# Kernel optimization log

Measured on AMD Instinct MI355X. Metric: run time of the kernel, lower is better.

The kernel has to match this reference:

```python
import jax, jax.numpy as jnp
import numpy as np

K = 4
TEMPERATURE = 30.0


def setup_inputs() -> dict:
    key = jax.random.key(0)
    ks = jax.random.split(key, 6)
    B, C, H, W_sp = 32, 128, 56, 56
    Cout, kh, kw = 128, 3, 3
    Cred = max(C // 4, 1)
    x = jax.random.normal(ks[0], (B, C, H, W_sp), dtype=jnp.float32)
    # K parallel conv kernels + biases (fan-in scaled init)
    fan = C * kh * kw
    W = jax.random.normal(ks[1], (K, Cout, C, kh, kw), dtype=jnp.float32) / np.sqrt(fan)
    b = jax.random.normal(ks[2], (K, Cout), dtype=jnp.float32) * 0.01
    # attention branch: 1x1 convs == dense on pooled features
    aw1 = jax.random.normal(ks[3], (Cred, C), dtype=jnp.float32) / np.sqrt(C)
    aw2 = jax.random.normal(ks[4], (K, Cred), dtype=jnp.float32) / np.sqrt(Cred)
    return {"x": x, "W": W, "b": b, "aw1": aw1, "aw2": aw2}


def reference(x, W, b, aw1, aw2):
    # attention: global avg pool -> 1x1 conv (dense) -> relu -> 1x1 conv -> softmax(logits/T)
    pooled = jnp.mean(x, axis=(2, 3))                       # [B, C]
    h1 = jax.nn.relu(jnp.einsum('bc,rc->br', pooled, aw1))  # [B, Cred]
    logits = jnp.einsum('br,kr->bk', h1, aw2)               # [B, K]
    attn = jax.nn.softmax(logits / TEMPERATURE, axis=1)     # [B, K]

    pad = 1
    out = None
    for i in range(K):  # fixed small K, structurally distinct kernels
        yi = jax.lax.conv_general_dilated(
            x, W[i], window_strides=(1, 1), padding=[(pad, pad), (pad, pad)],
            dimension_numbers=('NCHW', 'OIHW', 'NCHW'))
        yi = yi + b[i][None, :, None, None]
        yi = yi * attn[:, i][:, None, None, None]
        out = yi if out is None else out + yi
    return out
```

## Files before the change

kernel.cpp:

```cpp
#include <hip/hip_runtime.h>
#include <hip/hip_bf16.h>
#include <stdint.h>

typedef __bf16 bf16x8 __attribute__((ext_vector_type(8)));
typedef float  f32x4  __attribute__((ext_vector_type(4)));
typedef unsigned short u16x8 __attribute__((ext_vector_type(8)));
typedef unsigned int   u32x4 __attribute__((ext_vector_type(4)));

#define NB 32
#define NC 128
#define NH 56
#define NW 56
#define NK 4
#define NCO 128
#define NCR 32
#define NHW 3136
#define TEMPER 30.0f

#define WS_ATTN   0u
#define WS_BC     4096u
#define WS_ROWSUM 65536u
#define WS_WC     1048576u
#define WS_XT     10485760u

__global__ void xt_kernel(const float* __restrict__ x, __hip_bfloat16* __restrict__ xt,
                          float* __restrict__ rowsum) {
  __shared__ float lds[58 * 133];
  int xcd = blockIdx.x & 7;
  int j   = blockIdx.x >> 3;
  int b   = xcd * 4 + j / 58;
  int hp  = j % 58;
  int blk = b * 58 + hp;
  int h = hp - 1;
  bool hin = (h >= 0) && (h < NH);
  int tid = threadIdx.x;
  if (hin) {
    const float* xrow = x + ((size_t)b * NC) * NHW + (size_t)h * NW;
    for (int i = tid; i < 128 * 14; i += 256) {
      int c = i / 14;
      int w4 = (i - c * 14) * 4;
      float4 v = *(const float4*)(xrow + (size_t)c * NHW + w4);
      int base = (w4 + 1) * 133 + c;
      lds[base]         = v.x;
      lds[base + 133]   = v.y;
      lds[base + 2*133] = v.z;
      lds[base + 3*133] = v.w;
    }
  }
  __syncthreads();
  __hip_bfloat16* orow = xt + (size_t)blk * (58 * 128);
  for (int i = tid; i < 58 * 16; i += 256) {
    int wp = i >> 4;
    int cg = (i & 15) << 3;
    u16x8 o;
    if (!hin || wp == 0 || wp == 57) {
      o = (u16x8)0;
    } else {
      const float* src = lds + wp * 133 + cg;
      #pragma unroll
      for (int jx = 0; jx < 8; ++jx) {
        union { __hip_bfloat16 b; unsigned short u; } cv;
        cv.b = __float2bfloat16(src[jx]);
        o[jx] = cv.u;
      }
    }
    *(u16x8*)(orow + wp * 128 + cg) = o;
  }
  if (hin && tid < 128) {
    float s = 0.f;
    #pragma unroll 8
    for (int wp = 1; wp <= 56; ++wp) s += lds[wp * 133 + tid];
    rowsum[(size_t)blk * 128 + tid] = s;
  }
}

__global__ void attn_kernel(const float* __restrict__ rowsum, const float* __restrict__ aw1,
                            const float* __restrict__ aw2, const float* __restrict__ bias,
                            float* __restrict__ attn, float* __restrict__ bc_out) {
  int b = blockIdx.x;
  __shared__ float sp[NC], h1[NCR], at[NK];
  int t = threadIdx.x;
  if (t < NC) {
    float s = 0.f;
    for (int hp = 1; hp <= 56; ++hp) s += rowsum[((size_t)b * 58 + hp) * 128 + t];
    sp[t] = s * (1.0f / (float)NHW);
  }
  __syncthreads();
  if (t < NCR) {
    float s = 0.f;
    for (int c = 0; c < NC; ++c) s += aw1[t*NC + c] * sp[c];
    h1[t] = s > 0.f ? s : 0.f;
  }
  __syncthreads();
  if (t == 0) {
    float lg[NK], mx = -1e30f;
    for (int k = 0; k < NK; ++k) {
      float s = 0.f;
      for (int r = 0; r < NCR; ++r) s += aw2[k*NCR + r] * h1[r];
      lg[k] = s * (1.0f/TEMPER);
      mx = fmaxf(mx, lg[k]);
    }
    float den = 0.f, e[NK];
    for (int k = 0; k < NK; ++k) { e[k] = expf(lg[k]-mx); den += e[k]; }
    float inv = 1.0f/den;
    for (int k = 0; k < NK; ++k) { at[k] = e[k]*inv; attn[b*NK+k] = at[k]; }
  }
  __syncthreads();
  if (t < NCO) {
    float s = 0.f;
    for (int k = 0; k < NK; ++k) s += at[k] * bias[k*NCO + t];
    bc_out[b*NCO + t] = s;
  }
}

__global__ void combine_kernel(const float* __restrict__ W, const float* __restrict__ attn,
                               __hip_bfloat16* __restrict__ wc) {
  int gid = blockIdx.x;
  int bg  = gid >> 6;
  int tcell = (gid & 63) * 256 + threadIdx.x;
  int co = tcell >> 7, ci = tcell & 127;
  float w[4][9];
  const float* wp = W + ((size_t)co * 128 + ci) * 9;
  #pragma unroll
  for (int k = 0; k < 4; ++k)
    #pragma unroll
    for (int j = 0; j < 9; ++j)
      w[k][j] = wp[(size_t)k * 147456 + j];
  for (int b = bg * 8; b < bg * 8 + 8; ++b) {
    float a0 = attn[b*4+0], a1 = attn[b*4+1], a2 = attn[b*4+2], a3 = attn[b*4+3];
    #pragma unroll
    for (int j = 0; j < 9; ++j) {
      float v = a0*w[0][j] + a1*w[1][j] + a2*w[2][j] + a3*w[3][j];
      wc[(((size_t)b*9 + j) * 128 + co) * 128 + ci] = __float2bfloat16(v);
    }
  }
}

#define RS 2368
#define CS 40
#define BBUF (3072*8)
#define ABUF (1536*8)

__global__ __launch_bounds__(512, 2) void conv_kernel(
    const unsigned short* __restrict__ xt,
    const unsigned short* __restrict__ wc,
    const float* __restrict__ bc,
    float* __restrict__ out) {
  __shared__ __align__(16) unsigned short lds_a[2*ABUF];
  __shared__ __align__(16) unsigned short lds_b[2*BBUF];
  const int tid  = threadIdx.x;
  const int lane = tid & 63;
  const int wv   = tid >> 6;
  const int wm   = wv >> 2;
  const int wn   = wv & 3;
  const int bid  = blockIdx.x;
  const int xcd  = bid & 7;
  const int jj   = bid >> 3;
  const int b    = xcd*4 + jj/7;
  const int r0   = (jj % 7) * 8;
  const int li   = lane & 15;
  const int kg   = lane >> 4;

  int srcB[6];
  #pragma unroll
  for (int i = 0; i < 6; ++i) {
    int q = i*512 + tid;
    int r = q / 296;
    int sl = q - r*296;
    int col = sl / 5;
    int part = sl - col*5;
    int rc = r  > 9  ? 9  : r;
    int cl = col > 57 ? 57 : col;
    int pc = part > 3 ? 3 : part;
    srcB[i] = ((r0 + rc)*58 + cl)*128 + pc*8;
  }
  int srcA[3];
  #pragma unroll
  for (int i = 0; i < 3; ++i) {
    int c = i*512 + tid;
    int kwl  = c >> 9;
    int co   = (c & 511) >> 2;
    int part = c & 3;
    srcA[i] = (kwl*128 + co)*128 + part*8;
  }

  int xoff[7];
  #pragma unroll
  for (int f = 0; f < 7; ++f) {
    int pos = wn*112 + f*16 + li;
    int rB = pos / 56;
    int cB = pos - rB*56;
    xoff[f] = rB*RS + cB*CS + kg*8;
  }
  const int aRead = (wm*64 + li)*32 + kg*8;

  const f32x4 vzero = {0.f, 0.f, 0.f, 0.f};
  f32x4 acc[4][7];
  #pragma unroll
  for (int mo = 0; mo < 4; ++mo)
    #pragma unroll
    for (int f = 0; f < 7; ++f) acc[mo][f] = vzero;

  const unsigned short* xtg = xt + (size_t)b*(58*58*128);
  const unsigned short* wcg = wc + (size_t)b*(9*128*128);

  u32x4 aST[3], bST[6];

  #define LOAD_A(ccn, khn) do { \
    _Pragma("unroll") \
    for (int i = 0; i < 3; ++i) \
      aST[i] = *(const u32x4*)(wcg + (khn)*49152 + srcA[i] + (ccn)*32); \
  } while (0)

  #define LOAD_B(ccn) do { \
    _Pragma("unroll") \
    for (int i = 0; i < 6; ++i) \
      bST[i] = *(const u32x4*)(xtg + srcB[i] + (ccn)*32); \
  } while (0)

  #define WRITE_A(bufidx) do { \
    _Pragma("unroll") \
    for (int i = 0; i < 3; ++i) \
      *(u32x4*)(lds_a + (bufidx)*ABUF + (i*512 + tid)*8) = aST[i]; \
  } while (0)

  #define WRITE_B(bufidx) do { \
    _Pragma("unroll") \
    for (int i = 0; i < 6; ++i) \
      *(u32x4*)(lds_b + (bufidx)*BBUF + (i*512 + tid)*8) = bST[i]; \
  } while (0)

  #define COMPUTE(s, cc, kh) do { \
    const unsigned short* pa = lds_a + ((s)&1)*ABUF; \
    const unsigned short* pb = lds_b + ((cc)&1)*BBUF; \
    _Pragma("unroll") \
    for (int kwl = 0; kwl < 3; ++kwl) { \
      bf16x8 af[4], bf[7]; \
      _Pragma("unroll") \
      for (int mo = 0; mo < 4; ++mo) \
        af[mo] = *(const bf16x8*)(pa + kwl*4096 + aRead + mo*512); \
      _Pragma("unroll") \
      for (int f = 0; f < 7; ++f) \
        bf[f] = *(const bf16x8*)(pb + xoff[f] + (kh)*RS + kwl*CS); \
      __builtin_amdgcn_s_setprio(1); \
      _Pragma("unroll") \
      for (int mo = 0; mo < 4; ++mo) \
        _Pragma("unroll") \
        for (int f = 0; f < 7; ++f) \
          acc[mo][f] = __builtin_amdgcn_mfma_f32_16x16x32_bf16(af[mo], bf[f], acc[mo][f], 0, 0, 0); \
      __builtin_amdgcn_s_setprio(0); \
    } \
  } while (0)

  #define STEP(s, cc, kh) do { \
    if ((s) < 11) LOAD_A(((s)+1)/3, ((s)+1)%3); \
    if ((kh) == 0 && (cc) < 3) LOAD_B((cc)+1); \
    COMPUTE(s, cc, kh); \
    __syncthreads(); \
    if ((s) < 11) WRITE_A(((s)+1)&1); \
    if ((kh) == 0 && (cc) < 3) WRITE_B(((cc)+1)&1); \
    __syncthreads(); \
  } while (0)

  LOAD_A(0, 0);
  LOAD_B(0);
  WRITE_A(0);
  WRITE_B(0);
  __syncthreads();

  STEP(0,  0, 0);
  STEP(1,  0, 1);
  STEP(2,  0, 2);
  STEP(3,  1, 0);
  STEP(4,  1, 1);
  STEP(5,  1, 2);
  STEP(6,  2, 0);
  STEP(7,  2, 1);
  STEP(8,  2, 2);
  STEP(9,  3, 0);
  STEP(10, 3, 1);
  STEP(11, 3, 2);

  float* ob = out + (size_t)b*NCO*NHW;
  #pragma unroll
  for (int mo = 0; mo < 4; ++mo) {
    #pragma unroll
    for (int rg = 0; rg < 4; ++rg) {
      const int co = wm*64 + mo*16 + kg*4 + rg;
      const float bv = bc[b*NCO + co];
      float* orow = ob + (size_t)co*NHW;
      #pragma unroll
      for (int f = 0; f < 7; ++f) {
        int pos = wn*112 + f*16 + li;
        int rB = pos / 56;
        int cB = pos - rB*56;
        orow[(r0 + rB)*56 + cB] = acc[mo][f][rg] + bv;
      }
    }
  }
}

extern "C" void kernel_launch(void* const* d_in, const int* in_sizes, int n_in,
                              void* d_out, int out_size, void* d_ws, size_t ws_size,
                              hipStream_t stream) {
  const float* x   = (const float*)d_in[0];
  const float* W   = (const float*)d_in[1];
  const float* bia = (const float*)d_in[2];
  const float* aw1 = (const float*)d_in[3];
  const float* aw2 = (const float*)d_in[4];
  float* out = (float*)d_out;
  char* ws = (char*)d_ws;
  float* attn   = (float*)(ws + WS_ATTN);
  float* bcm    = (float*)(ws + WS_BC);
  float* rowsum = (float*)(ws + WS_ROWSUM);
  __hip_bfloat16* wc = (__hip_bfloat16*)(ws + WS_WC);
  __hip_bfloat16* xt = (__hip_bfloat16*)(ws + WS_XT);

  xt_kernel<<<NB*58, 256, 0, stream>>>(x, xt, rowsum);
  attn_kernel<<<NB, 128, 0, stream>>>(rowsum, aw1, aw2, bia, attn, bcm);
  combine_kernel<<<256, 256, 0, stream>>>(W, attn, wc);
  conv_kernel<<<224, 512, 0, stream>>>((const unsigned short*)xt,
                                       (const unsigned short*)wc, bcm, out);
}
```

Before: 67.41 us.

## Add producer warps staging tiles via global_load_lds for warp-specialized conv

Adds two dedicated producer wavefronts to the conv block. They copy weight and input tiles straight from global memory into LDS using global_load_lds, while the 8 compute wavefronts only run MFMA. This removes the register round-trip and the extra barrier that the old design spent staging loads through VGPRs. The cost is that only 2 waves handle all loads, there is one sync per step, and launch bounds change to 640 threads with one block per CU, which may lower occupancy.

New measurement: 110.8 us. +64.4%, slower.

```diff
diff --git a/kernel.cpp b/kernel.cpp
--- a/kernel.cpp
+++ b/kernel.cpp
@@ -5,7 +5,6 @@
 typedef __bf16 bf16x8 __attribute__((ext_vector_type(8)));
 typedef float  f32x4  __attribute__((ext_vector_type(4)));
 typedef unsigned short u16x8 __attribute__((ext_vector_type(8)));
-typedef unsigned int   u32x4 __attribute__((ext_vector_type(4)));
 
 #define NB 32
 #define NC 128
@@ -138,10 +137,15 @@
 
 #define RS 2368
 #define CS 40
-#define BBUF (3072*8)
-#define ABUF (1536*8)
-
-__global__ __launch_bounds__(512, 2) void conv_kernel(
+#define ABUF 12288
+#define BBUF 24576
+
+#define GLOAD16(src, dst) \
+  __builtin_amdgcn_global_load_lds( \
+    (const __attribute__((address_space(1))) unsigned int*)(src), \
+    (__attribute__((address_space(3))) unsigned int*)(dst), 16, 0, 0)
+
+__global__ __launch_bounds__(640, 1) void conv_kernel(
     const unsigned short* __restrict__ xt,
     const unsigned short* __restrict__ wc,
     const float* __restrict__ bc,
@@ -151,8 +155,6 @@
   const int tid  = threadIdx.x;
   const int lane = tid & 63;
   const int wv   = tid >> 6;
-  const int wm   = wv >> 2;
-  const int wn   = wv & 3;
   const int bid  = blockIdx.x;
   const int xcd  = bid & 7;
   const int jj   = bid >> 3;
@@ -161,29 +163,38 @@
   const int li   = lane & 15;
   const int kg   = lane >> 4;
 
-  int srcB[6];
-  #pragma unroll
-  for (int i = 0; i < 6; ++i) {
-    int q = i*512 + tid;
-    int r = q / 296;
-    int sl = q - r*296;
-    int col = sl / 5;
-    int part = sl - col*5;
-    int rc = r  > 9  ? 9  : r;
-    int cl = col > 57 ? 57 : col;
-    int pc = part > 3 ? 3 : part;
-    srcB[i] = ((r0 + rc)*58 + cl)*128 + pc*8;
-  }
-  int srcA[3];
-  #pragma unroll
-  for (int i = 0; i < 3; ++i) {
-    int c = i*512 + tid;
-    int kwl  = c >> 9;
-    int co   = (c & 511) >> 2;
-    int part = c & 3;
-    srcA[i] = (kwl*128 + co)*128 + part*8;
-  }
-
+  const unsigned short* xtg = xt + (size_t)b*(58*58*128);
+  const unsigned short* wcg = wc + (size_t)b*(9*128*128);
+
+  const int ptid = tid - 512;
+  const int pw   = wv - 8;
+  int srcA[12];
+  int srcB[24];
+  if (tid >= 512) {
+    #pragma unroll
+    for (int i = 0; i < 12; ++i) {
+      int c = i*128 + ptid;
+      int kwl  = c >> 9;
+      int co   = (c & 511) >> 2;
+      int part = c & 3;
+      srcA[i] = (kwl*128 + co)*128 + part*8;
+    }
+    #pragma unroll
+    for (int i = 0; i < 24; ++i) {
+      int q = i*128 + ptid;
+      int r = q / 296;
+      int sl = q - r*296;
+      int col = sl / 5;
+      int part = sl - col*5;
+      int rc = r  > 9  ? 9  : r;
+      int cl = col > 57 ? 57 : col;
+      int pc = part > 3 ? 3 : part;
+      srcB[i] = ((r0 + rc)*58 + cl)*128 + pc*8;
+    }
+  }
+
+  const int wm = wv >> 2;
+  const int wn = wv & 3;
   int xoff[7];
   #pragma unroll
   for (int f = 0; f < 7; ++f) {
@@ -201,33 +212,18 @@
     #pragma unroll
     for (int f = 0; f < 7; ++f) acc[mo][f] = vzero;
 
-  const unsigned short* xtg = xt + (size_t)b*(58*58*128);
-  const unsigned short* wcg = wc + (size_t)b*(9*128*128);
-
-  u32x4 aST[3], bST[6];
-
-  #define LOAD_A(ccn, khn) do { \
+  #define STAGE_A(bufidx, ccn, khn) do { \
+    unsigned short* dbase = lds_a + (bufidx)*ABUF + (pw*64)*8; \
     _Pragma("unroll") \
-    for (int i = 0; i < 3; ++i) \
-      aST[i] = *(const u32x4*)(wcg + (khn)*49152 + srcA[i] + (ccn)*32); \
+    for (int i = 0; i < 12; ++i) \
+      GLOAD16(wcg + (khn)*49152 + srcA[i] + (ccn)*32, dbase + i*1024); \
   } while (0)
 
-  #define LOAD_B(ccn) do { \
+  #define STAGE_B(bufidx, ccn) do { \
+    unsigned short* dbase = lds_b + (bufidx)*BBUF + (pw*64)*8; \
     _Pragma("unroll") \
-    for (int i = 0; i < 6; ++i) \
-      bST[i] = *(const u32x4*)(xtg + srcB[i] + (ccn)*32); \
-  } while (0)
-
-  #define WRITE_A(bufidx) do { \
-    _Pragma("unroll") \
-    for (int i = 0; i < 3; ++i) \
-      *(u32x4*)(lds_a + (bufidx)*ABUF + (i*512 + tid)*8) = aST[i]; \
-  } while (0)
-
-  #define WRITE_B(bufidx) do { \
-    _Pragma("unroll") \
-    for (int i = 0; i < 6; ++i) \
-      *(u32x4*)(lds_b + (bufidx)*BBUF + (i*512 + tid)*8) = bST[i]; \
+    for (int i = 0; i < 24; ++i) \
+      GLOAD16(xtg + srcB[i] + (ccn)*32, dbase + i*1024); \
   } while (0)
 
   #define COMPUTE(s, cc, kh) do { \
@@ -253,19 +249,19 @@
   } while (0)
 
   #define STEP(s, cc, kh) do { \
-    if ((s) < 11) LOAD_A(((s)+1)/3, ((s)+1)%3); \
-    if ((kh) == 0 && (cc) < 3) LOAD_B((cc)+1); \
-    COMPUTE(s, cc, kh); \
-    __syncthreads(); \
-    if ((s) < 11) WRITE_A(((s)+1)&1); \
-    if ((kh) == 0 && (cc) < 3) WRITE_B(((cc)+1)&1); \
+    if (tid >= 512) { \
+      if ((s) < 11) STAGE_A(((s)+1)&1, ((s)+1)/3, ((s)+1)%3); \
+      if ((kh) == 0 && (cc) < 3) STAGE_B(((cc)+1)&1, (cc)+1); \
+    } else { \
+      COMPUTE(s, cc, kh); \
+    } \
     __syncthreads(); \
   } while (0)
 
-  LOAD_A(0, 0);
-  LOAD_B(0);
-  WRITE_A(0);
-  WRITE_B(0);
+  if (tid >= 512) {
+    STAGE_A(0, 0, 0);
+    STAGE_B(0, 0);
+  }
   __syncthreads();
 
   STEP(0,  0, 0);
@@ -281,20 +277,22 @@
   STEP(10, 3, 1);
   STEP(11, 3, 2);
 
-  float* ob = out + (size_t)b*NCO*NHW;
-  #pragma unroll
-  for (int mo = 0; mo < 4; ++mo) {
-    #pragma unroll
-    for (int rg = 0; rg < 4; ++rg) {
-      const int co = wm*64 + mo*16 + kg*4 + rg;
-      const float bv = bc[b*NCO + co];
-      float* orow = ob + (size_t)co*NHW;
+  if (tid < 512) {
+    float* ob = out + (size_t)b*NCO*NHW;
+    #pragma unroll
+    for (int mo = 0; mo < 4; ++mo) {
       #pragma unroll
-      for (int f = 0; f < 7; ++f) {
-        int pos = wn*112 + f*16 + li;
-        int rB = pos / 56;
-        int cB = pos - rB*56;
-        orow[(r0 + rB)*56 + cB] = acc[mo][f][rg] + bv;
+      for (int rg = 0; rg < 4; ++rg) {
+        const int co = wm*64 + mo*16 + kg*4 + rg;
+        const float bv = bc[b*NCO + co];
+        float* orow = ob + (size_t)co*NHW;
+        #pragma unroll
+        for (int f = 0; f < 7; ++f) {
+          int pos = wn*112 + f*16 + li;
+          int rB = pos / 56;
+          int cB = pos - rB*56;
+          orow[(r0 + rB)*56 + cB] = acc[mo][f][rg] + bv;
+        }
       }
     }
   }
@@ -319,6 +317,6 @@
   xt_kernel<<<NB*58, 256, 0, stream>>>(x, xt, rowsum);
   attn_kernel<<<NB, 128, 0, stream>>>(rowsum, aw1, aw2, bia, attn, bcm);
   combine_kernel<<<256, 256, 0, stream>>>(W, attn, wc);
-  conv_kernel<<<224, 512, 0, stream>>>((const unsigned short*)xt,
+  conv_kernel<<<224, 640, 0, stream>>>((const unsigned short*)xt,
                                        (const unsigned short*)wc, bcm, out);
 }
```
